# Optimization experiments

Measured on AMD Instinct MI355X. Metric: run time of the kernel, lower is better.

## Reference

```python
import jax, jax.numpy as jnp
import numpy as np
from jax import lax

H = 32  # hidden size


def _lstm_layer(x, Wih, Whh, bih, bhh):
    """x: [B, T, D_in]; returns [B, T, H]. PyTorch gate order i,f,g,o."""
    B = x.shape[0]
    b = bih + bhh  # [4H]
    # precompute input projections for all timesteps: [T, B, 4H]
    xp = jnp.einsum('btd,gd->tbg', x, Wih) + b

    def step(carry, xt):
        h, c = carry
        gates = xt + h @ Whh.T  # [B, 4H]
        i, f, g, o = jnp.split(gates, 4, axis=-1)
        i = jax.nn.sigmoid(i)
        f = jax.nn.sigmoid(f)
        g = jnp.tanh(g)
        o = jax.nn.sigmoid(o)
        c = f * c + i * g
        h = o * jnp.tanh(c)
        return (h, c), h

    init = (jnp.zeros((B, H), x.dtype), jnp.zeros((B, H), x.dtype))
    _, ys = lax.scan(step, init, xp)  # ys: [T, B, H]
    return jnp.swapaxes(ys, 0, 1)


def _lstm5(x, Wih0, Wih_rest, Whh, bih, bhh):
    h = _lstm_layer(x, Wih0, Whh[0], bih[0], bhh[0])
    for l in range(4):  # fixed small layer count
        h = _lstm_layer(h, Wih_rest[l], Whh[l + 1], bih[l + 1], bhh[l + 1])
    return h


def setup_inputs() -> dict:
    key = jax.random.key(0)
    ks = jax.random.split(key, 18)
    s = 1.0 / np.sqrt(H)
    B, T = 16384, 20
    u = lambda k, shp: jax.random.uniform(k, shp, jnp.float32, -s, s)
    return {
        'accel': jax.random.normal(ks[0], (B, T, 3), jnp.float32),
        'gyro': jax.random.normal(ks[1], (B, T, 3), jnp.float32),
        'accel_Wih0': u(ks[2], (4 * H, 3)),
        'accel_Wih_rest': u(ks[3], (4, 4 * H, H)),
        'accel_Whh': u(ks[4], (5, 4 * H, H)),
        'accel_bih': u(ks[5], (5, 4 * H)),
        'accel_bhh': u(ks[6], (5, 4 * H)),
        'gyro_Wih0': u(ks[7], (4 * H, 3)),
        'gyro_Wih_rest': u(ks[8], (4, 4 * H, H)),
        'gyro_Whh': u(ks[9], (5, 4 * H, H)),
        'gyro_bih': u(ks[10], (5, 4 * H)),
        'gyro_bhh': u(ks[11], (5, 4 * H)),
        'fc1_w': u(ks[12], (128, T * H * 2)),
        'fc1_b': u(ks[13], (128,)),
        'fc2_w': u(ks[14], (5, 128)),
        'fc2_b': u(ks[15], (5,)),
    }


def reference(accel, gyro, accel_Wih0, accel_Wih_rest, accel_Whh, accel_bih,
              accel_bhh, gyro_Wih0, gyro_Wih_rest, gyro_Whh, gyro_bih,
              gyro_bhh, fc1_w, fc1_b, fc2_w, fc2_b):
    a = _lstm5(accel, accel_Wih0, accel_Wih_rest, accel_Whh, accel_bih, accel_bhh)
    g = _lstm5(gyro, gyro_Wih0, gyro_Wih_rest, gyro_Whh, gyro_bih, gyro_bhh)
    x = jnp.concatenate([a, g], axis=1)          # [B, 2T, H]
    x = x.reshape(x.shape[0], -1)                # [B, 2*T*H]
    x = jax.nn.relu(x @ fc1_w.T + fc1_b)         # [B, 128]
    return x @ fc2_w.T + fc2_b                   # [B, 5]
```

## Files before the change

### kernel.cpp

```cpp
#include <hip/hip_runtime.h>
#include <math.h>

#define B_TOTAL 16384
#define T_STEPS 20
#define NGRP    1024

typedef __attribute__((ext_vector_type(8))) __bf16 bf16x8;
typedef __attribute__((ext_vector_type(4))) float f32x4;

__device__ __forceinline__ float sigf(float x) {
    return __builtin_amdgcn_rcpf(1.0f + __expf(-x));
}
__device__ __forceinline__ float tanhf_fast(float x) {
    return fmaf(-2.0f, __builtin_amdgcn_rcpf(__expf(2.0f * x) + 1.0f), 1.0f);
}

__device__ __forceinline__ __bf16 bf16_bits(unsigned short s) {
    __bf16 r; __builtin_memcpy(&r, &s, 2); return r;
}
__device__ __forceinline__ void split_trunc(float x, __bf16& hi, __bf16& lo) {
    unsigned u = __float_as_uint(x);
    hi = bf16_bits((unsigned short)(u >> 16));
    float l = x - __uint_as_float(u & 0xFFFF0000u);
    lo = bf16_bits((unsigned short)(__float_as_uint(l) >> 16));
}

__global__ __launch_bounds__(256, 4)
void lstm5_mfma(const float* __restrict__ accel, const float* __restrict__ gyro,
                const float* __restrict__ aWih0, const float* __restrict__ aWihR,
                const float* __restrict__ aWhh,  const float* __restrict__ aBih,
                const float* __restrict__ aBhh,
                const float* __restrict__ gWih0, const float* __restrict__ gWihR,
                const float* __restrict__ gWhh,  const float* __restrict__ gBih,
                const float* __restrict__ gBhh,
                const __bf16* __restrict__ w1ah, const __bf16* __restrict__ w1al,
                float* __restrict__ Zpart ) {
    const int tid  = threadIdx.x;
    const int w    = tid >> 6;
    const int lane = tid & 63;
    const int e    = lane & 15;
    const int quad = lane >> 4;
    const int sensor = blockIdx.y;
    const int bbase  = blockIdx.x * 16;

    const float* xin  = sensor ? gyro  : accel;
    const float* Wih0 = sensor ? gWih0 : aWih0;
    const float* WihR = sensor ? gWihR : aWihR;
    const float* Whh  = sensor ? gWhh  : aWhh;
    const float* Bih  = sensor ? gBih  : aBih;
    const float* Bhh  = sensor ? gBhh  : aBhh;

    __shared__ __align__(16) __bf16 shi[20 * 512];
    __shared__ __align__(16) __bf16 slo[20 * 512];

    const int ug0 = w * 8 + quad;
    const int ug1 = w * 8 + 4 + quad;

    const int m_row   = lane & 15;
    const int orow_t0 = (m_row & 3) * 32 + (w * 8 + (m_row >> 2));
    const int orow_t1 = (m_row & 3) * 32 + (w * 8 + 4 + (m_row >> 2));

    bf16x8 wih_h0, wih_l0, wih_h1, wih_l1;
    bf16x8 whh_h0, whh_l0, whh_h1, whh_l1;
    f32x4  bias0v, bias1v;
    float  c0 = 0.f, c1 = 0.f;

#define LOAD_FRAG(Wsrc, orow, fh, fl)                         \
    {                                                         \
        const float* p_ = (Wsrc) + (orow) * 32 + quad * 8;    \
        _Pragma("unroll")                                     \
        for (int jj = 0; jj < 8; ++jj) {                      \
            __bf16 h_, l_;                                    \
            split_trunc(p_[jj], h_, l_);                      \
            (fh)[jj] = h_;  (fl)[jj] = l_;                    \
        }                                                     \
    }

#define LOAD_BIAS(l)                                                        \
    {                                                                       \
        _Pragma("unroll")                                                   \
        for (int r = 0; r < 4; ++r) {                                       \
            bias0v[r] = Bih[(l) * 128 + r * 32 + ug0] + Bhh[(l) * 128 + r * 32 + ug0]; \
            bias1v[r] = Bih[(l) * 128 + r * 32 + ug1] + Bhh[(l) * 128 + r * 32 + ug1]; \
        }                                                                   \
    }

#define ACT_STORE(t)                                                        \
    {                                                                       \
        float i0 = sigf(acc0[0]), f0 = sigf(acc0[1]);                       \
        float g0 = tanhf_fast(acc0[2]), o0 = sigf(acc0[3]);                 \
        c0 = f0 * c0 + i0 * g0;                                             \
        float h0 = o0 * tanhf_fast(c0);                                     \
        float i1 = sigf(acc1[0]), f1 = sigf(acc1[1]);                       \
        float g1 = tanhf_fast(acc1[2]), o1 = sigf(acc1[3]);                 \
        c1 = f1 * c1 + i1 * g1;                                             \
        float h1 = o1 * tanhf_fast(c1);                                     \
        __syncthreads();             \
        int i0x = (t) * 512 + w * 128 + e * 8 + quad;                       \
        int i1x = i0x + 4;                                                  \
        __bf16 hh_, ll_;                                                    \
        split_trunc(h0, hh_, ll_);  shi[i0x] = hh_;  slo[i0x] = ll_;        \
        split_trunc(h1, hh_, ll_);  shi[i1x] = hh_;  slo[i1x] = ll_;        \
        __syncthreads();       \
    }

    {
        LOAD_FRAG(Whh, orow_t0, whh_h0, whh_l0);
        LOAD_FRAG(Whh, orow_t1, whh_h1, whh_l1);
        LOAD_BIAS(0);
        float w0reg[2][4][3];
#pragma unroll
        for (int r = 0; r < 4; ++r)
#pragma unroll
            for (int k = 0; k < 3; ++k) {
                w0reg[0][r][k] = Wih0[(r * 32 + ug0) * 3 + k];
                w0reg[1][r][k] = Wih0[(r * 32 + ug1) * 3 + k];
            }
        const float* xrow = xin + (size_t)(bbase + e) * (T_STEPS * 3);

        for (int t = 0; t < T_STEPS; ++t) {
            float x0 = xrow[t * 3 + 0];
            float x1 = xrow[t * 3 + 1];
            float x2 = xrow[t * 3 + 2];
            f32x4 acc0 = bias0v;
            f32x4 acc1 = bias1v;
#pragma unroll
            for (int r = 0; r < 4; ++r) {
                acc0[r] = fmaf(w0reg[0][r][0], x0,
                          fmaf(w0reg[0][r][1], x1,
                          fmaf(w0reg[0][r][2], x2, acc0[r])));
                acc1[r] = fmaf(w0reg[1][r][0], x0,
                          fmaf(w0reg[1][r][1], x1,
                          fmaf(w0reg[1][r][2], x2, acc1[r])));
            }
            if (t > 0) {
                int rb = (t - 1) * 512 + quad * 128 + e * 8;
                bf16x8 bh = *(const bf16x8*)&shi[rb];
                bf16x8 bl = *(const bf16x8*)&slo[rb];
                acc0 = __builtin_amdgcn_mfma_f32_16x16x32_bf16(whh_h0, bh, acc0, 0, 0, 0);
                acc0 = __builtin_amdgcn_mfma_f32_16x16x32_bf16(whh_h0, bl, acc0, 0, 0, 0);
                acc0 = __builtin_amdgcn_mfma_f32_16x16x32_bf16(whh_l0, bh, acc0, 0, 0, 0);
                acc1 = __builtin_amdgcn_mfma_f32_16x16x32_bf16(whh_h1, bh, acc1, 0, 0, 0);
                acc1 = __builtin_amdgcn_mfma_f32_16x16x32_bf16(whh_h1, bl, acc1, 0, 0, 0);
                acc1 = __builtin_amdgcn_mfma_f32_16x16x32_bf16(whh_l1, bh, acc1, 0, 0, 0);
            }
            ACT_STORE(t);
        }
    }

    for (int l = 1; l < 5; ++l) {
        const float* Wi = WihR + (l - 1) * 4096;
        const float* Wh = Whh + l * 4096;
        LOAD_FRAG(Wi, orow_t0, wih_h0, wih_l0);
        LOAD_FRAG(Wi, orow_t1, wih_h1, wih_l1);
        LOAD_FRAG(Wh, orow_t0, whh_h0, whh_l0);
        LOAD_FRAG(Wh, orow_t1, whh_h1, whh_l1);
        LOAD_BIAS(l);
        c0 = 0.f; c1 = 0.f;

        for (int t = 0; t < T_STEPS; ++t) {
            f32x4 acc0, acc1;
            {
                int rb = t * 512 + quad * 128 + e * 8;
                bf16x8 bh = *(const bf16x8*)&shi[rb];
                bf16x8 bl = *(const bf16x8*)&slo[rb];
                acc0 = __builtin_amdgcn_mfma_f32_16x16x32_bf16(wih_h0, bh, bias0v, 0, 0, 0);
                acc0 = __builtin_amdgcn_mfma_f32_16x16x32_bf16(wih_h0, bl, acc0, 0, 0, 0);
                acc0 = __builtin_amdgcn_mfma_f32_16x16x32_bf16(wih_l0, bh, acc0, 0, 0, 0);
                acc1 = __builtin_amdgcn_mfma_f32_16x16x32_bf16(wih_h1, bh, bias1v, 0, 0, 0);
                acc1 = __builtin_amdgcn_mfma_f32_16x16x32_bf16(wih_h1, bl, acc1, 0, 0, 0);
                acc1 = __builtin_amdgcn_mfma_f32_16x16x32_bf16(wih_l1, bh, acc1, 0, 0, 0);
            }
            if (t > 0) {
                int rb = (t - 1) * 512 + quad * 128 + e * 8;
                bf16x8 bh = *(const bf16x8*)&shi[rb];
                bf16x8 bl = *(const bf16x8*)&slo[rb];
                acc0 = __builtin_amdgcn_mfma_f32_16x16x32_bf16(whh_h0, bh, acc0, 0, 0, 0);
                acc0 = __builtin_amdgcn_mfma_f32_16x16x32_bf16(whh_h0, bl, acc0, 0, 0, 0);
                acc0 = __builtin_amdgcn_mfma_f32_16x16x32_bf16(whh_l0, bh, acc0, 0, 0, 0);
                acc1 = __builtin_amdgcn_mfma_f32_16x16x32_bf16(whh_h1, bh, acc1, 0, 0, 0);
                acc1 = __builtin_amdgcn_mfma_f32_16x16x32_bf16(whh_h1, bl, acc1, 0, 0, 0);
                acc1 = __builtin_amdgcn_mfma_f32_16x16x32_bf16(whh_l1, bh, acc1, 0, 0, 0);
            }
            ACT_STORE(t);
        }
    }
    __syncthreads();

    {
        f32x4 zacc0 = (f32x4){0.f, 0.f, 0.f, 0.f};
        f32x4 zacc1 = (f32x4){0.f, 0.f, 0.f, 0.f};
        const int mt0 = w * 2, mt1 = w * 2 + 1;
        for (int t = 0; t < T_STEPS; ++t) {
            int rb = t * 512 + quad * 128 + e * 8;
            bf16x8 bh = *(const bf16x8*)&shi[rb];
            bf16x8 bl = *(const bf16x8*)&slo[rb];
            int ks = sensor * 20 + t;
            size_t ab0 = ((size_t)((mt0 * 40 + ks) * 64 + lane)) * 8;
            size_t ab1 = ((size_t)((mt1 * 40 + ks) * 64 + lane)) * 8;
            bf16x8 ah0 = *(const bf16x8*)(w1ah + ab0);
            bf16x8 al0 = *(const bf16x8*)(w1al + ab0);
            bf16x8 ah1 = *(const bf16x8*)(w1ah + ab1);
            bf16x8 al1 = *(const bf16x8*)(w1al + ab1);
            zacc0 = __builtin_amdgcn_mfma_f32_16x16x32_bf16(ah0, bh, zacc0, 0, 0, 0);
            zacc0 = __builtin_amdgcn_mfma_f32_16x16x32_bf16(ah0, bl, zacc0, 0, 0, 0);
            zacc0 = __builtin_amdgcn_mfma_f32_16x16x32_bf16(al0, bh, zacc0, 0, 0, 0);
            zacc1 = __builtin_amdgcn_mfma_f32_16x16x32_bf16(ah1, bh, zacc1, 0, 0, 0);
            zacc1 = __builtin_amdgcn_mfma_f32_16x16x32_bf16(ah1, bl, zacc1, 0, 0, 0);
            zacc1 = __builtin_amdgcn_mfma_f32_16x16x32_bf16(al1, bh, zacc1, 0, 0, 0);
        }
        float* zp = Zpart + ((size_t)(sensor * NGRP + blockIdx.x)) * 2048;
#pragma unroll
        for (int r = 0; r < 4; ++r) {
            zp[mt0 * 256 + (quad * 4 + r) * 16 + e] = zacc0[r];
            zp[mt1 * 256 + (quad * 4 + r) * 16 + e] = zacc1[r];
        }
    }
#undef LOAD_FRAG
#undef LOAD_BIAS
#undef ACT_STORE
}

__global__ void w1_prep(const float* __restrict__ w1,
                        __bf16* __restrict__ w1ah, __bf16* __restrict__ w1al) {
    int t = blockIdx.x * blockDim.x + threadIdx.x;
    if (t >= 20480) return;
    int lane = t & 63;
    int ks   = (t >> 6) % 40;
    int mt   = t / (64 * 40);
    int row  = mt * 16 + (lane & 15);
    int col0 = ks * 32 + (lane >> 4) * 8;
    const float* src = w1 + row * 1280 + col0;
#pragma unroll
    for (int j = 0; j < 8; ++j) {
        __bf16 h_, l_;
        split_trunc(src[j], h_, l_);
        w1ah[t * 8 + j] = h_;
        w1al[t * 8 + j] = l_;
    }
}

__global__ __launch_bounds__(256, 8)
void fc_finish(const float* __restrict__ Zpart, const float* __restrict__ fc1_b,
               const float* __restrict__ fc2_w, const float* __restrict__ fc2_b,
               float* __restrict__ out) {
    const int tid = threadIdx.x;
    const int e   = tid & 15;
    const int rt  = tid >> 4;
    const int g   = blockIdx.x;
    __shared__ float sp[16][16][5];

    const float* z0 = Zpart + (size_t)g * 2048;
    const float* z1 = Zpart + (size_t)(NGRP + g) * 2048;
    float p[5] = {0.f, 0.f, 0.f, 0.f, 0.f};
#pragma unroll
    for (int rr = 0; rr < 8; ++rr) {
        int row = rt * 8 + rr;
        int zi  = (row >> 4) * 256 + (row & 15) * 16 + e;
        float v = fmaxf(z0[zi] + z1[zi] + fc1_b[row], 0.f);
#pragma unroll
        for (int n = 0; n < 5; ++n) p[n] = fmaf(v, fc2_w[n * 128 + row], p[n]);
    }
#pragma unroll
    for (int n = 0; n < 5; ++n) sp[rt][e][n] = p[n];
    __syncthreads();
    if (tid < 80) {
        int col = tid / 5, n = tid - col * 5;
        float s = fc2_b[n];
#pragma unroll
        for (int k = 0; k < 16; ++k) s += sp[k][col][n];
        out[(size_t)(g * 16 + col) * 5 + n] = s;
    }
}

extern "C" void kernel_launch(void* const* d_in, const int* in_sizes, int n_in,
                              void* d_out, int out_size, void* d_ws, size_t ws_size,
                              hipStream_t stream) {
    const float* accel  = (const float*)d_in[0];
    const float* gyro   = (const float*)d_in[1];
    const float* aWih0  = (const float*)d_in[2];
    const float* aWihR  = (const float*)d_in[3];
    const float* aWhh   = (const float*)d_in[4];
    const float* aBih   = (const float*)d_in[5];
    const float* aBhh   = (const float*)d_in[6];
    const float* gWih0  = (const float*)d_in[7];
    const float* gWihR  = (const float*)d_in[8];
    const float* gWhh   = (const float*)d_in[9];
    const float* gBih   = (const float*)d_in[10];
    const float* gBhh   = (const float*)d_in[11];
    const float* fc1_w  = (const float*)d_in[12];
    const float* fc1_b  = (const float*)d_in[13];
    const float* fc2_w  = (const float*)d_in[14];
    const float* fc2_b  = (const float*)d_in[15];
    float* out = (float*)d_out;

    __bf16* W1ah = (__bf16*)d_ws;
    __bf16* W1al = W1ah + 163840;
    float*  Zpart = (float*)(W1al + 163840);

    hipLaunchKernelGGL(w1_prep, dim3(80), dim3(256), 0, stream, fc1_w, W1ah, W1al);

    hipLaunchKernelGGL(lstm5_mfma, dim3(NGRP, 2), dim3(256), 0, stream,
                       accel, gyro, aWih0, aWihR, aWhh, aBih, aBhh,
                       gWih0, gWihR, gWhh, gBih, gBhh, W1ah, W1al, Zpart);

    hipLaunchKernelGGL(fc_finish, dim3(NGRP), dim3(256), 0, stream,
                       Zpart, fc1_b, fc2_w, fc2_b, out);
}
```

Baseline: 292.6 us.

## Fold log2e scaling into weights and fuse FC tail via atomic counter

```diff
diff --git a/kernel.cpp b/kernel.cpp
--- a/kernel.cpp
+++ b/kernel.cpp
@@ -5,14 +5,21 @@
 #define T_STEPS 20
 #define NGRP    1024
 
+#define LOG2E    1.44269504088896f
+#define TWOLOG2E 2.88539008177793f
+
 typedef __attribute__((ext_vector_type(8))) __bf16 bf16x8;
 typedef __attribute__((ext_vector_type(4))) float f32x4;
 
-__device__ __forceinline__ float sigf(float x) {
-    return __builtin_amdgcn_rcpf(1.0f + __expf(-x));
-}
-__device__ __forceinline__ float tanhf_fast(float x) {
-    return fmaf(-2.0f, __builtin_amdgcn_rcpf(__expf(2.0f * x) + 1.0f), 1.0f);
+__device__ __forceinline__ float sig2(float xp) {
+    return __builtin_amdgcn_rcpf(1.0f + __builtin_exp2f(-xp));
+}
+__device__ __forceinline__ float tanh2pre(float xp) {
+    return fmaf(-2.0f, __builtin_amdgcn_rcpf(__builtin_exp2f(xp) + 1.0f), 1.0f);
+}
+__device__ __forceinline__ float tanh2(float c) {
+    return fmaf(-2.0f,
+                __builtin_amdgcn_rcpf(__builtin_exp2f(c * TWOLOG2E) + 1.0f), 1.0f);
 }
 
 __device__ __forceinline__ __bf16 bf16_bits(unsigned short s) {
@@ -34,7 +41,10 @@
                 const float* __restrict__ gWhh,  const float* __restrict__ gBih,
                 const float* __restrict__ gBhh,
                 const __bf16* __restrict__ w1ah, const __bf16* __restrict__ w1al,
-                float* __restrict__ Zpart ) {
+                float* __restrict__ Zpart ,
+                int* __restrict__ cnt ,
+                const float* __restrict__ fc1_b, const float* __restrict__ fc2_w,
+                const float* __restrict__ fc2_b, float* __restrict__ out) {
     const int tid  = threadIdx.x;
     const int w    = tid >> 6;
     const int lane = tid & 63;
@@ -52,6 +62,7 @@
 
     __shared__ __align__(16) __bf16 shi[20 * 512];
     __shared__ __align__(16) __bf16 slo[20 * 512];
+    __shared__ int sflag;
 
     const int ug0 = w * 8 + quad;
     const int ug1 = w * 8 + 4 + quad;
@@ -59,6 +70,7 @@
     const int m_row   = lane & 15;
     const int orow_t0 = (m_row & 3) * 32 + (w * 8 + (m_row >> 2));
     const int orow_t1 = (m_row & 3) * 32 + (w * 8 + 4 + (m_row >> 2));
+    const float sA = ((m_row & 3) == 2) ? TWOLOG2E : LOG2E;
 
     bf16x8 wih_h0, wih_l0, wih_h1, wih_l1;
     bf16x8 whh_h0, whh_l0, whh_h1, whh_l1;
@@ -71,7 +83,7 @@
         _Pragma("unroll")                                     \
         for (int jj = 0; jj < 8; ++jj) {                      \
             __bf16 h_, l_;                                    \
-            split_trunc(p_[jj], h_, l_);                      \
+            split_trunc(p_[jj] * sA, h_, l_);                 \
             (fh)[jj] = h_;  (fl)[jj] = l_;                    \
         }                                                     \
     }
@@ -80,21 +92,22 @@
     {                                                                       \
         _Pragma("unroll")                                                   \
         for (int r = 0; r < 4; ++r) {                                       \
-            bias0v[r] = Bih[(l) * 128 + r * 32 + ug0] + Bhh[(l) * 128 + r * 32 + ug0]; \
-            bias1v[r] = Bih[(l) * 128 + r * 32 + ug1] + Bhh[(l) * 128 + r * 32 + ug1]; \
+            float sc = (r == 2) ? TWOLOG2E : LOG2E;                         \
+            bias0v[r] = (Bih[(l) * 128 + r * 32 + ug0] + Bhh[(l) * 128 + r * 32 + ug0]) * sc; \
+            bias1v[r] = (Bih[(l) * 128 + r * 32 + ug1] + Bhh[(l) * 128 + r * 32 + ug1]) * sc; \
         }                                                                   \
     }
 
 #define ACT_STORE(t)                                                        \
     {                                                                       \
-        float i0 = sigf(acc0[0]), f0 = sigf(acc0[1]);                       \
-        float g0 = tanhf_fast(acc0[2]), o0 = sigf(acc0[3]);                 \
+        float i0 = sig2(acc0[0]), f0 = sig2(acc0[1]);                       \
+        float g0 = tanh2pre(acc0[2]), o0 = sig2(acc0[3]);                   \
         c0 = f0 * c0 + i0 * g0;                                             \
-        float h0 = o0 * tanhf_fast(c0);                                     \
-        float i1 = sigf(acc1[0]), f1 = sigf(acc1[1]);                       \
-        float g1 = tanhf_fast(acc1[2]), o1 = sigf(acc1[3]);                 \
+        float h0 = o0 * tanh2(c0);                                          \
+        float i1 = sig2(acc1[0]), f1 = sig2(acc1[1]);                       \
+        float g1 = tanh2pre(acc1[2]), o1 = sig2(acc1[3]);                   \
         c1 = f1 * c1 + i1 * g1;                                             \
-        float h1 = o1 * tanhf_fast(c1);                                     \
+        float h1 = o1 * tanh2(c1);                                          \
         __syncthreads();             \
         int i0x = (t) * 512 + w * 128 + e * 8 + quad;                       \
         int i1x = i0x + 4;                                                  \
@@ -110,12 +123,14 @@
         LOAD_BIAS(0);
         float w0reg[2][4][3];
 #pragma unroll
-        for (int r = 0; r < 4; ++r)
+        for (int r = 0; r < 4; ++r) {
+            float sc = (r == 2) ? TWOLOG2E : LOG2E;
 #pragma unroll
             for (int k = 0; k < 3; ++k) {
-                w0reg[0][r][k] = Wih0[(r * 32 + ug0) * 3 + k];
-                w0reg[1][r][k] = Wih0[(r * 32 + ug1) * 3 + k];
-            }
+                w0reg[0][r][k] = Wih0[(r * 32 + ug0) * 3 + k] * sc;
+                w0reg[1][r][k] = Wih0[(r * 32 + ug1) * 3 + k] * sc;
+            }
+        }
         const float* xrow = xin + (size_t)(bbase + e) * (T_STEPS * 3);
 
         for (int t = 0; t < T_STEPS; ++t) {
@@ -191,6 +206,7 @@
         f32x4 zacc0 = (f32x4){0.f, 0.f, 0.f, 0.f};
         f32x4 zacc1 = (f32x4){0.f, 0.f, 0.f, 0.f};
         const int mt0 = w * 2, mt1 = w * 2 + 1;
+#pragma unroll 2
         for (int t = 0; t < T_STEPS; ++t) {
             int rb = t * 512 + quad * 128 + e * 8;
             bf16x8 bh = *(const bf16x8*)&shi[rb];
@@ -216,14 +232,47 @@
             zp[mt1 * 256 + (quad * 4 + r) * 16 + e] = zacc1[r];
         }
     }
+
+    __threadfence();
+    __syncthreads();
+    if (tid == 0) sflag = atomicAdd(&cnt[blockIdx.x], 1);
+    __syncthreads();
+    if (sflag == 1) {
+        __threadfence();
+        float* sp = (float*)shi;
+        const float* z0 = Zpart + (size_t)blockIdx.x * 2048;
+        const float* z1 = Zpart + (size_t)(NGRP + blockIdx.x) * 2048;
+        const int e2 = tid & 15, rt = tid >> 4;
+        float p[5] = {0.f, 0.f, 0.f, 0.f, 0.f};
+#pragma unroll
+        for (int rr = 0; rr < 8; ++rr) {
+            int row = rt * 8 + rr;
+            int zi  = (row >> 4) * 256 + (row & 15) * 16 + e2;
+            float v = fmaxf(z0[zi] + z1[zi] + fc1_b[row], 0.f);
+#pragma unroll
+            for (int n = 0; n < 5; ++n) p[n] = fmaf(v, fc2_w[n * 128 + row], p[n]);
+        }
+#pragma unroll
+        for (int n = 0; n < 5; ++n) sp[(rt * 16 + e2) * 5 + n] = p[n];
+        __syncthreads();
+        if (tid < 80) {
+            int col = tid / 5, n = tid - col * 5;
+            float s = fc2_b[n];
+#pragma unroll
+            for (int k = 0; k < 16; ++k) s += sp[(k * 16 + col) * 5 + n];
+            out[(size_t)(blockIdx.x * 16 + col) * 5 + n] = s;
+        }
+    }
 #undef LOAD_FRAG
 #undef LOAD_BIAS
 #undef ACT_STORE
 }
 
 __global__ void w1_prep(const float* __restrict__ w1,
-                        __bf16* __restrict__ w1ah, __bf16* __restrict__ w1al) {
+                        __bf16* __restrict__ w1ah, __bf16* __restrict__ w1al,
+                        int* __restrict__ cnt) {
     int t = blockIdx.x * blockDim.x + threadIdx.x;
+    if (t < NGRP) cnt[t] = 0;
     if (t >= 20480) return;
     int lane = t & 63;
     int ks   = (t >> 6) % 40;
@@ -237,39 +286,6 @@
         split_trunc(src[j], h_, l_);
         w1ah[t * 8 + j] = h_;
         w1al[t * 8 + j] = l_;
-    }
-}
-
-__global__ __launch_bounds__(256, 8)
-void fc_finish(const float* __restrict__ Zpart, const float* __restrict__ fc1_b,
-               const float* __restrict__ fc2_w, const float* __restrict__ fc2_b,
-               float* __restrict__ out) {
-    const int tid = threadIdx.x;
-    const int e   = tid & 15;
-    const int rt  = tid >> 4;
-    const int g   = blockIdx.x;
-    __shared__ float sp[16][16][5];
-
-    const float* z0 = Zpart + (size_t)g * 2048;
-    const float* z1 = Zpart + (size_t)(NGRP + g) * 2048;
-    float p[5] = {0.f, 0.f, 0.f, 0.f, 0.f};
-#pragma unroll
-    for (int rr = 0; rr < 8; ++rr) {
-        int row = rt * 8 + rr;
-        int zi  = (row >> 4) * 256 + (row & 15) * 16 + e;
-        float v = fmaxf(z0[zi] + z1[zi] + fc1_b[row], 0.f);
-#pragma unroll
-        for (int n = 0; n < 5; ++n) p[n] = fmaf(v, fc2_w[n * 128 + row], p[n]);
-    }
-#pragma unroll
-    for (int n = 0; n < 5; ++n) sp[rt][e][n] = p[n];
-    __syncthreads();
-    if (tid < 80) {
-        int col = tid / 5, n = tid - col * 5;
-        float s = fc2_b[n];
-#pragma unroll
-        for (int k = 0; k < 16; ++k) s += sp[k][col][n];
-        out[(size_t)(g * 16 + col) * 5 + n] = s;
     }
 }
 
@@ -294,16 +310,16 @@
     const float* fc2_b  = (const float*)d_in[15];
     float* out = (float*)d_out;
 
-    __bf16* W1ah = (__bf16*)d_ws;
-    __bf16* W1al = W1ah + 163840;
+    __bf16* W1ah  = (__bf16*)d_ws;
+    __bf16* W1al  = W1ah + 163840;
     float*  Zpart = (float*)(W1al + 163840);
-
-    hipLaunchKernelGGL(w1_prep, dim3(80), dim3(256), 0, stream, fc1_w, W1ah, W1al);
+    int*    cnt   = (int*)(Zpart + (size_t)2 * NGRP * 2048);
+
+    hipLaunchKernelGGL(w1_prep, dim3(80), dim3(256), 0, stream,
+                       fc1_w, W1ah, W1al, cnt);
 
     hipLaunchKernelGGL(lstm5_mfma, dim3(NGRP, 2), dim3(256), 0, stream,
                        accel, gyro, aWih0, aWihR, aWhh, aBih, aBhh,
-                       gWih0, gWihR, gWhh, gBih, gBhh, W1ah, W1al, Zpart);
-
-    hipLaunchKernelGGL(fc_finish, dim3(NGRP), dim3(256), 0, stream,
-                       Zpart, fc1_b, fc2_w, fc2_b, out);
-}
+                       gWih0, gWihR, gWhh, gBih, gBhh,
+                       W1ah, W1al, Zpart, cnt, fc1_b, fc2_w, fc2_b, out);
+}
```

Measured after the change: 519.9 us. 1.78x slower.
